# Kernel optimization log

Measured on AMD Instinct MI355X. Metric: run time of the kernel, lower is better.

The kernel has to match this reference:

```python
import jax, jax.numpy as jnp
import numpy as np

B, S, C, L = 32, 256, 50, 20   # batch, max_seq_len, char_emb_dim, word_len
F, W = 30, 3                   # filter_num, char_window_size


def setup_inputs() -> dict:
    key = jax.random.key(0)
    k1, k2, k3 = jax.random.split(key, 3)
    char_embeddings_feature = jax.random.normal(k1, (B, S, C, L), dtype=jnp.float32)
    # torch grouped Conv1d weight: [out_ch=C*F, in_ch/groups=1, kernel=W]
    weight = jax.random.normal(k2, (C * F, 1, W), dtype=jnp.float32) * 0.1
    bias = jax.random.normal(k3, (C * F,), dtype=jnp.float32) * 0.1
    return {"char_embeddings_feature": char_embeddings_feature, "weight": weight, "bias": bias}


def reference(char_embeddings_feature, weight, bias):
    b, s, c, l = char_embeddings_feature.shape
    out_ch = weight.shape[0]
    # Fuse the per-position python loop: fold (batch, seq) into one conv batch dim.
    x = char_embeddings_feature.reshape(b * s, c, l)
    # Grouped (depthwise-style) conv: groups == c, each group has F output filters.
    y = jax.lax.conv_general_dilated(
        x, weight,
        window_strides=(1,), padding='VALID',
        dimension_numbers=('NCH', 'OIH', 'NCH'),
        feature_group_count=c,
    )  # [b*s, c*F, l-W+1]
    y = y + bias[None, :, None]
    # max-pool over conv output length, then restore (batch, seq)
    return y.max(axis=2).reshape(b, s, out_ch)
```

## Files before the change

kernel.cpp:

```cpp
#include <hip/hip_runtime.h>

constexpr int Bc = 32;
constexpr int Sc = 256;
constexpr int Cc = 50;
constexpr int Lc = 20;
constexpr int Fc = 30;
constexpr int Wc = 3;
constexpr int OUT_CH   = Cc * Fc;
constexpr int CONV_LEN = Lc - Wc + 1;
constexpr int XSZ      = Cc * Lc;
constexpr int BLOCK    = 256;

__global__ __launch_bounds__(BLOCK)
void charcnn_kernel(const float* __restrict__ x,
                    const float* __restrict__ weight,
                    const float* __restrict__ bias,
                    float* __restrict__ out)
{
    __shared__ float xs[XSZ];

    const int bs = blockIdx.x;
    const float* xp = x + (size_t)bs * XSZ;

    for (int i = threadIdx.x; i < XSZ; i += BLOCK)
        xs[i] = xp[i];
    __syncthreads();

    float* op = out + (size_t)bs * OUT_CH;

    for (int o = threadIdx.x; o < OUT_CH; o += BLOCK) {
        const int c = o / Fc;
        const float w0 = weight[o * Wc + 0];
        const float w1 = weight[o * Wc + 1];
        const float w2 = weight[o * Wc + 2];

        const float4* rowv = (const float4*)(xs + c * Lc);
        float v[Lc];
        #pragma unroll
        for (int i = 0; i < Lc / 4; ++i) {
            const float4 q = rowv[i];
            v[4 * i + 0] = q.x;
            v[4 * i + 1] = q.y;
            v[4 * i + 2] = q.z;
            v[4 * i + 3] = q.w;
        }

        float m = -INFINITY;
        #pragma unroll
        for (int p = 0; p < CONV_LEN; ++p) {
            const float conv = fmaf(v[p], w0, fmaf(v[p + 1], w1, v[p + 2] * w2));
            m = fmaxf(m, conv);
        }
        op[o] = m + bias[o];
    }
}

extern "C" void kernel_launch(void* const* d_in, const int* in_sizes, int n_in,
                              void* d_out, int out_size, void* d_ws, size_t ws_size,
                              hipStream_t stream) {
    const float* x      = (const float*)d_in[0];
    const float* weight = (const float*)d_in[1];
    const float* bias   = (const float*)d_in[2];
    float* out          = (float*)d_out;

    const int nPos = Bc * Sc;
    charcnn_kernel<<<nPos, BLOCK, 0, stream>>>(x, weight, bias, out);
}
```

Before: 31.61 us.

## Compute six output channels per thread with register-reused input row

Each thread now handles six consecutive output filters of one input channel, loading the 20-element row from shared memory once and reusing it across six weight sets. The shared-memory fill becomes a single float4 copy per thread, and weights, biases and outputs use float2 vector accesses. A max-pairs reduction and a launch_bounds occupancy hint are added. Only 250 of the 256 threads do compute, and per-thread register use rises.

```diff
diff --git a/kernel.cpp b/kernel.cpp
--- a/kernel.cpp
+++ b/kernel.cpp
@@ -10,8 +10,9 @@
 constexpr int CONV_LEN = Lc - Wc + 1;
 constexpr int XSZ      = Cc * Lc;
 constexpr int BLOCK    = 256;
+constexpr int CH_PER_T = 6;
 
-__global__ __launch_bounds__(BLOCK)
+__global__ __launch_bounds__(BLOCK, 4)
 void charcnn_kernel(const float* __restrict__ x,
                     const float* __restrict__ weight,
                     const float* __restrict__ bias,
@@ -20,39 +21,73 @@
     __shared__ float xs[XSZ];
 
     const int bs = blockIdx.x;
-    const float* xp = x + (size_t)bs * XSZ;
+    const int t  = threadIdx.x;
 
-    for (int i = threadIdx.x; i < XSZ; i += BLOCK)
-        xs[i] = xp[i];
+    {
+        const float4* src = (const float4*)(x + (size_t)bs * XSZ);
+        float4*       dst = (float4*)xs;
+        if (t < XSZ / 4) dst[t] = src[t];
+    }
     __syncthreads();
 
-    float* op = out + (size_t)bs * OUT_CH;
+    if (t >= OUT_CH / CH_PER_T) return;
 
-    for (int o = threadIdx.x; o < OUT_CH; o += BLOCK) {
-        const int c = o / Fc;
-        const float w0 = weight[o * Wc + 0];
-        const float w1 = weight[o * Wc + 1];
-        const float w2 = weight[o * Wc + 2];
+    const int c = t / 5;
 
+    float v[Lc];
+    {
         const float4* rowv = (const float4*)(xs + c * Lc);
-        float v[Lc];
         #pragma unroll
         for (int i = 0; i < Lc / 4; ++i) {
             const float4 q = rowv[i];
-            v[4 * i + 0] = q.x;
-            v[4 * i + 1] = q.y;
-            v[4 * i + 2] = q.z;
-            v[4 * i + 3] = q.w;
+            v[4*i+0] = q.x; v[4*i+1] = q.y; v[4*i+2] = q.z; v[4*i+3] = q.w;
         }
+    }
 
-        float m = -INFINITY;
+    float w[CH_PER_T * Wc];
+    {
+        const float2* wp = (const float2*)(weight + t * (CH_PER_T * Wc));
         #pragma unroll
-        for (int p = 0; p < CONV_LEN; ++p) {
-            const float conv = fmaf(v[p], w0, fmaf(v[p + 1], w1, v[p + 2] * w2));
-            m = fmaxf(m, conv);
+        for (int i = 0; i < (CH_PER_T * Wc) / 2; ++i) {
+            const float2 q = wp[i];
+            w[2*i] = q.x; w[2*i+1] = q.y;
         }
-        op[o] = m + bias[o];
     }
+    float bb[CH_PER_T];
+    {
+        const float2* bp = (const float2*)(bias + t * CH_PER_T);
+        #pragma unroll
+        for (int i = 0; i < CH_PER_T / 2; ++i) {
+            const float2 q = bp[i];
+            bb[2*i] = q.x; bb[2*i+1] = q.y;
+        }
+    }
+
+    float res[CH_PER_T];
+    #pragma unroll
+    for (int j = 0; j < CH_PER_T; ++j) {
+        const float w0 = w[3*j + 0];
+        const float w1 = w[3*j + 1];
+        const float w2 = w[3*j + 2];
+
+        float cv[CONV_LEN];
+        #pragma unroll
+        for (int p = 0; p < CONV_LEN; ++p)
+            cv[p] = fmaf(v[p], w0, fmaf(v[p+1], w1, v[p+2] * w2));
+
+        float m = fmaxf(fmaxf(cv[0], cv[1]), cv[2]);
+        #pragma unroll
+        for (int p = 3; p + 1 < CONV_LEN; p += 2)
+            m = fmaxf(fmaxf(m, cv[p]), cv[p+1]);
+        m = fmaxf(m, cv[CONV_LEN - 1]);
+
+        res[j] = m + bb[j];
+    }
+
+    float* op = out + (size_t)bs * OUT_CH + t * CH_PER_T;
+    #pragma unroll
+    for (int i = 0; i < CH_PER_T / 2; ++i)
+        ((float2*)op)[i] = make_float2(res[2*i], res[2*i+1]);
 }
 
 extern "C" void kernel_launch(void* const* d_in, const int* in_sizes, int n_in,
```

Result: faster. 29.09 us (-8.0%).
